# Kernel tuning notes

Measured on AMD Instinct MI355X. Metric: run time of the kernel, lower is better.

Reference implementation:

```python
import jax, jax.numpy as jnp
import numpy as np


def setup_inputs() -> dict:
    key = jax.random.key(0)
    k1, k2 = jax.random.split(key)
    B, N, M = 4, 8192, 8192
    rec = jax.random.normal(k1, (B, N, 3), dtype=jnp.float32)
    data = jax.random.normal(k2, (B, M, 3), dtype=jnp.float32)
    return {"rec": rec, "data": data}


def reference(rec, data):
    # Squared pairwise Euclidean distances: (B, N, M)
    x2 = jnp.sum(rec * rec, axis=-1)          # (B, N)
    y2 = jnp.sum(data * data, axis=-1)        # (B, M)
    xy = jnp.einsum('bnd,bmd->bnm', rec, data)  # (B, N, M)
    d = x2[:, :, None] + y2[:, None, :] - 2.0 * xy
    d = jnp.maximum(d, 0.0)
    rec_dist = jnp.min(d, axis=2)   # (B, N): nearest data point for each rec point
    data_dist = jnp.min(d, axis=1)  # (B, M): nearest rec point for each data point
    # Chamfer: per-batch max of the two directed mean distances, then batch mean
    per_batch = jnp.maximum(jnp.mean(rec_dist, axis=1), jnp.mean(data_dist, axis=1))
    return jnp.mean(per_batch)
```

## Files before the change

kernel.cpp:

```cpp
#include <hip/hip_runtime.h>

typedef float f32x16 __attribute__((ext_vector_type(16)));
typedef short bf16x8 __attribute__((ext_vector_type(8)));

constexpr int SROWS  = 256;
constexpr int NSLICE = 4;

__device__ inline short f2bf(float x) {
    unsigned u = __float_as_uint(x);
    unsigned r = (u + 0x7fffu + ((u >> 16) & 1u)) >> 16;
    return (short)r;
}
__device__ inline float bf2f(short h) {
    return __uint_as_float(((unsigned)(unsigned short)h) << 16);
}
__device__ inline float vmin16(f32x16 v) {
    float a = fminf(fminf(v[0], v[1]), fminf(v[2], v[3]));
    float b = fminf(fminf(v[4], v[5]), fminf(v[6], v[7]));
    float c = fminf(fminf(v[8], v[9]), fminf(v[10], v[11]));
    float d = fminf(fminf(v[12], v[13]), fminf(v[14], v[15]));
    return fminf(fminf(a, b), fminf(c, d));
}

__global__ __launch_bounds__(256)
void chamfer_prep(const float* __restrict__ rec, const float* __restrict__ data,
                  bf16x8* __restrict__ Ar, bf16x8* __restrict__ Br,
                  bf16x8* __restrict__ Ad, bf16x8* __restrict__ Bd,
                  int N, int M, int B)
{
    const int i = blockIdx.x * 256 + threadIdx.x;
    const int tot0 = B * N, tot = tot0 + B * M;
    if (i >= tot) return;
    const short ONE = 0x3F80;
    const bool isRec = i < tot0;
    const int j = isRec ? i : i - tot0;
    const float* p = (isRec ? rec : data) + (size_t)j * 3;
    const float x = p[0], y = p[1], z = p[2];
    const float w = fmaf(x, x, fmaf(y, y, z * z));
    const short hx = f2bf(x), hy = f2bf(y), hz = f2bf(z);
    const float fx = bf2f(hx), fy = bf2f(hy), fz = bf2f(hz);
    const short nhx = f2bf(-2.f * fx), nhy = f2bf(-2.f * fy), nhz = f2bf(-2.f * fz);
    const short nlx = f2bf(-2.f * (x - fx));
    const short nly = f2bf(-2.f * (y - fy));
    const short nlz = f2bf(-2.f * (z - fz));
    const short lx = f2bf(x - fx), ly = f2bf(y - fy), lz = f2bf(z - fz);
    const short wh = f2bf(w);
    const short wl = f2bf(w - bf2f(wh));

    bf16x8 A0 = {nhx, nhy, nhz, nlx, nly, nlz, wh, wl};
    bf16x8 A1 = {nhx, nhy, nhz, ONE, ONE, 0, 0, 0};
    bf16x8 B0 = {hx, hy, hz, hx, hy, hz, ONE, ONE};
    bf16x8 B1 = {lx, ly, lz, wh, wl, 0, 0, 0};

    bf16x8* Adst = (isRec ? Ar : Ad) + 2 * (size_t)j;
    bf16x8* Bdst = (isRec ? Br : Bd) + 2 * (size_t)j;
    Adst[0] = A0; Adst[1] = A1;
    Bdst[0] = B0; Bdst[1] = B1;
}

__global__ __launch_bounds__(256, 4)
void chamfer_mfma_kernel(const bf16x8* __restrict__ Ar, const bf16x8* __restrict__ Bd,
                         const bf16x8* __restrict__ Ad, const bf16x8* __restrict__ Br,
                         float* __restrict__ part_data,
                         float* __restrict__ part_rec,
                         int N, int M, int B)
{
    const int nSB1 = N / SROWS;
    const int G1   = B * nSB1 * NSLICE;

    const bf16x8* Ap; const bf16x8* Bp; float* outp;
    int S, T, idx;
    if ((int)blockIdx.x < G1) {
        Ap = Ar; Bp = Bd; outp = part_data; S = N; T = M; idx = blockIdx.x;
    } else {
        Ap = Ad; Bp = Br; outp = part_rec;  S = M; T = N; idx = blockIdx.x - G1;
    }
    const int nSB = S / SROWS;
    const int sl  = idx % NSLICE; idx /= NSLICE;
    const int sb  = idx % nSB;
    const int b   = idx / nSB;

    const int lane = threadIdx.x & 63, wave = threadIdx.x >> 6;
    const int c = lane & 31, h = lane >> 5;

    const bf16x8* __restrict__ Ab = Ap + 2 * ((size_t)b * S + sb * SROWS);
    const bf16x8* __restrict__ Bb = Bp + 2 * ((size_t)b * T);
    float* __restrict__ outBase = outp + ((size_t)b * nSB + sb) * T;

    bf16x8 a[8];
    #pragma unroll
    for (int f = 0; f < 8; ++f) a[f] = Ab[2 * (f * 32 + c) + h];

    f32x16 zacc;
    #pragma unroll
    for (int r = 0; r < 16; ++r) zacc[r] = 0.f;

    const int TS32 = (T / NSLICE) >> 5;
    const int t0   = sl * TS32 + wave;
    const int tEnd = (sl + 1) * TS32;

    bf16x8 bcur = Bb[2 * ((size_t)t0 * 32 + c) + h];
    for (int t = t0; t < tEnd; t += 4) {
        int tn = t + 4; if (tn >= tEnd) tn = t0;
        bf16x8 bnext = Bb[2 * ((size_t)tn * 32 + c) + h];

        f32x16 d0 = __builtin_amdgcn_mfma_f32_32x32x16_bf16(a[0], bcur, zacc, 0, 0, 0);
        f32x16 d1 = __builtin_amdgcn_mfma_f32_32x32x16_bf16(a[1], bcur, zacc, 0, 0, 0);
        float m0 = fminf(vmin16(d0), vmin16(d1));
        f32x16 d2 = __builtin_amdgcn_mfma_f32_32x32x16_bf16(a[2], bcur, zacc, 0, 0, 0);
        f32x16 d3 = __builtin_amdgcn_mfma_f32_32x32x16_bf16(a[3], bcur, zacc, 0, 0, 0);
        float m1 = fminf(vmin16(d2), vmin16(d3));
        f32x16 d4 = __builtin_amdgcn_mfma_f32_32x32x16_bf16(a[4], bcur, zacc, 0, 0, 0);
        f32x16 d5 = __builtin_amdgcn_mfma_f32_32x32x16_bf16(a[5], bcur, zacc, 0, 0, 0);
        float m2 = fminf(vmin16(d4), vmin16(d5));
        f32x16 d6 = __builtin_amdgcn_mfma_f32_32x32x16_bf16(a[6], bcur, zacc, 0, 0, 0);
        f32x16 d7 = __builtin_amdgcn_mfma_f32_32x32x16_bf16(a[7], bcur, zacc, 0, 0, 0);
        float m3 = fminf(vmin16(d6), vmin16(d7));

        float cm = fminf(fminf(m0, m1), fminf(m2, m3));
        cm = fminf(cm, __shfl_xor(cm, 32));
        if (lane < 32)
            outBase[(size_t)t * 32 + c] = cm;
        bcur = bnext;
    }
}

__global__ __launch_bounds__(256)
void chamfer_stage2(const float* __restrict__ part_data,
                    const float* __restrict__ part_rec,
                    float* __restrict__ bsums, int N, int M, int B)
{
    __shared__ float wsum[4];
    const int gid = blockIdx.x * 256 + threadIdx.x;
    const int nD = B * M;

    const float* base; size_t stride; int depth;
    if (gid < nD) {
        const int b = gid / M, col = gid - b * M;
        base = part_data + ((size_t)b * (N / SROWS)) * M + col;
        stride = M; depth = N / SROWS;
    } else {
        const int g = gid - nD;
        const int b = g / N, col = g - b * N;
        base = part_rec + ((size_t)b * (M / SROWS)) * N + col;
        stride = N; depth = M / SROWS;
    }
    float m0 = 3.4e38f, m1 = 3.4e38f, m2 = 3.4e38f, m3 = 3.4e38f;
    int s = 0;
    for (; s + 4 <= depth; s += 4) {
        m0 = fminf(m0, base[(s + 0) * stride]);
        m1 = fminf(m1, base[(s + 1) * stride]);
        m2 = fminf(m2, base[(s + 2) * stride]);
        m3 = fminf(m3, base[(s + 3) * stride]);
    }
    for (; s < depth; ++s) m0 = fminf(m0, base[s * stride]);
    float d = fmaxf(fminf(fminf(m0, m1), fminf(m2, m3)), 0.f);

    for (int off = 32; off; off >>= 1) d += __shfl_down(d, off);
    if ((threadIdx.x & 63) == 0) wsum[threadIdx.x >> 6] = d;
    __syncthreads();
    if (threadIdx.x == 0)
        bsums[blockIdx.x] = wsum[0] + wsum[1] + wsum[2] + wsum[3];
}

__global__ __launch_bounds__(256)
void chamfer_finalize(const float* __restrict__ bsums, float* __restrict__ out,
                      int N, int M, int B)
{
    __shared__ float smem[512];
    __shared__ float seg[16];
    const int ncD = M >> 8, ncR = N >> 8;
    const int nD  = B * ncD, ntot = nD + B * ncR;
    const int tid = threadIdx.x;
    for (int i = tid; i < ntot; i += 256) smem[i] = bsums[i];
    __syncthreads();
    if (tid < 2 * B) {
        const int dir = tid / B, bb = tid % B;
        float s = 0.f;
        if (dir == 0) for (int i = 0; i < ncD; ++i) s += smem[bb * ncD + i];
        else          for (int i = 0; i < ncR; ++i) s += smem[nD + bb * ncR + i];
        seg[tid] = s;
    }
    __syncthreads();
    if (tid == 0) {
        float acc = 0.f;
        for (int bb = 0; bb < B; ++bb)
            acc += fmaxf(seg[B + bb] / (float)N, seg[bb] / (float)M);
        out[0] = acc / (float)B;
    }
}

extern "C" void kernel_launch(void* const* d_in, const int* in_sizes, int n_in,
                              void* d_out, int out_size, void* d_ws, size_t ws_size,
                              hipStream_t stream)
{
    const float* rec  = (const float*)d_in[0];
    const float* data = (const float*)d_in[1];
    const int B = 4;
    const int N = in_sizes[0] / (B * 3);
    const int M = in_sizes[1] / (B * 3);
    const int tot = B * (N + M);

    char* w = (char*)d_ws;
    bf16x8* Ar = (bf16x8*)w;  w += (size_t)B * N * 2 * sizeof(bf16x8);
    bf16x8* Br = (bf16x8*)w;  w += (size_t)B * N * 2 * sizeof(bf16x8);
    bf16x8* Ad = (bf16x8*)w;  w += (size_t)B * M * 2 * sizeof(bf16x8);
    bf16x8* Bd = (bf16x8*)w;  w += (size_t)B * M * 2 * sizeof(bf16x8);
    float* part_data = (float*)w;  w += (size_t)B * (N / SROWS) * M * sizeof(float);
    float* part_rec  = (float*)w;  w += (size_t)B * (M / SROWS) * N * sizeof(float);
    float* bsums = (float*)w;

    chamfer_prep<<<(tot + 255) / 256, 256, 0, stream>>>(rec, data, Ar, Br, Ad, Bd,
                                                        N, M, B);
    const int G = B * (N / SROWS) * NSLICE + B * (M / SROWS) * NSLICE;
    chamfer_mfma_kernel<<<G, 256, 0, stream>>>(Ar, Bd, Ad, Br,
                                               part_data, part_rec, N, M, B);
    chamfer_stage2<<<tot / 256, 256, 0, stream>>>(part_data, part_rec, bsums,
                                                  N, M, B);
    chamfer_finalize<<<1, 256, 0, stream>>>(bsums, (float*)d_out, N, M, B);
}
```

Measured before the change: 48.60 us.

## Halve row tile and slices, reduce min elementwise before horizontal reduce

Each block now holds 128 source rows (four MFMA A fragments instead of eight) and the target range is split into two slices instead of four. This keeps the grid size unchanged while each wave runs a longer loop with fewer MFMAs per iteration. The min reduction now combines the MFMA outputs elementwise first and then does a single horizontal reduction written as three-input min chains, to cut VALU min work per MFMA. Partial-output writes and stage-2 depth double because there are twice as many source blocks, and each loaded B fragment is reused across fewer A rows.

```diff
diff --git a/kernel.cpp b/kernel.cpp
--- a/kernel.cpp
+++ b/kernel.cpp
@@ -3,8 +3,8 @@
 typedef float f32x16 __attribute__((ext_vector_type(16)));
 typedef short bf16x8 __attribute__((ext_vector_type(8)));
 
-constexpr int SROWS  = 256;
-constexpr int NSLICE = 4;
+constexpr int SROWS  = 128;
+constexpr int NSLICE = 2;
 
 __device__ inline short f2bf(float x) {
     unsigned u = __float_as_uint(x);
@@ -14,12 +14,15 @@
 __device__ inline float bf2f(short h) {
     return __uint_as_float(((unsigned)(unsigned short)h) << 16);
 }
-__device__ inline float vmin16(f32x16 v) {
-    float a = fminf(fminf(v[0], v[1]), fminf(v[2], v[3]));
-    float b = fminf(fminf(v[4], v[5]), fminf(v[6], v[7]));
-    float c = fminf(fminf(v[8], v[9]), fminf(v[10], v[11]));
-    float d = fminf(fminf(v[12], v[13]), fminf(v[14], v[15]));
-    return fminf(fminf(a, b), fminf(c, d));
+__device__ inline float vmin16_t(f32x16 v) {
+    float t1 = fminf(fminf(v[0], v[1]), v[2]);
+    float t2 = fminf(fminf(v[3], v[4]), v[5]);
+    float t3 = fminf(fminf(v[6], v[7]), v[8]);
+    float t4 = fminf(fminf(v[9], v[10]), v[11]);
+    float t5 = fminf(fminf(v[12], v[13]), v[14]);
+    float u1 = fminf(fminf(t1, t2), t3);
+    float u2 = fminf(fminf(t4, t5), v[15]);
+    return fminf(u1, u2);
 }
 
 __global__ __launch_bounds__(256)
@@ -87,9 +90,10 @@
     const bf16x8* __restrict__ Bb = Bp + 2 * ((size_t)b * T);
     float* __restrict__ outBase = outp + ((size_t)b * nSB + sb) * T;
 
-    bf16x8 a[8];
-    #pragma unroll
-    for (int f = 0; f < 8; ++f) a[f] = Ab[2 * (f * 32 + c) + h];
+    bf16x8 a0 = Ab[2 * (0 * 32 + c) + h];
+    bf16x8 a1 = Ab[2 * (1 * 32 + c) + h];
+    bf16x8 a2 = Ab[2 * (2 * 32 + c) + h];
+    bf16x8 a3 = Ab[2 * (3 * 32 + c) + h];
 
     f32x16 zacc;
     #pragma unroll
@@ -104,20 +108,18 @@
         int tn = t + 4; if (tn >= tEnd) tn = t0;
         bf16x8 bnext = Bb[2 * ((size_t)tn * 32 + c) + h];
 
-        f32x16 d0 = __builtin_amdgcn_mfma_f32_32x32x16_bf16(a[0], bcur, zacc, 0, 0, 0);
-        f32x16 d1 = __builtin_amdgcn_mfma_f32_32x32x16_bf16(a[1], bcur, zacc, 0, 0, 0);
-        float m0 = fminf(vmin16(d0), vmin16(d1));
-        f32x16 d2 = __builtin_amdgcn_mfma_f32_32x32x16_bf16(a[2], bcur, zacc, 0, 0, 0);
-        f32x16 d3 = __builtin_amdgcn_mfma_f32_32x32x16_bf16(a[3], bcur, zacc, 0, 0, 0);
-        float m1 = fminf(vmin16(d2), vmin16(d3));
-        f32x16 d4 = __builtin_amdgcn_mfma_f32_32x32x16_bf16(a[4], bcur, zacc, 0, 0, 0);
-        f32x16 d5 = __builtin_amdgcn_mfma_f32_32x32x16_bf16(a[5], bcur, zacc, 0, 0, 0);
-        float m2 = fminf(vmin16(d4), vmin16(d5));
-        f32x16 d6 = __builtin_amdgcn_mfma_f32_32x32x16_bf16(a[6], bcur, zacc, 0, 0, 0);
-        f32x16 d7 = __builtin_amdgcn_mfma_f32_32x32x16_bf16(a[7], bcur, zacc, 0, 0, 0);
-        float m3 = fminf(vmin16(d6), vmin16(d7));
-
-        float cm = fminf(fminf(m0, m1), fminf(m2, m3));
+        f32x16 d0 = __builtin_amdgcn_mfma_f32_32x32x16_bf16(a0, bcur, zacc, 0, 0, 0);
+        f32x16 d1 = __builtin_amdgcn_mfma_f32_32x32x16_bf16(a1, bcur, zacc, 0, 0, 0);
+        f32x16 acc;
+        #pragma unroll
+        for (int r = 0; r < 16; ++r) acc[r] = fminf(d0[r], d1[r]);
+        f32x16 d2 = __builtin_amdgcn_mfma_f32_32x32x16_bf16(a2, bcur, zacc, 0, 0, 0);
+        f32x16 d3 = __builtin_amdgcn_mfma_f32_32x32x16_bf16(a3, bcur, zacc, 0, 0, 0);
+        #pragma unroll
+        for (int r = 0; r < 16; ++r)
+            acc[r] = fminf(fminf(d2[r], d3[r]), acc[r]);
+
+        float cm = vmin16_t(acc);
         cm = fminf(cm, __shfl_xor(cm, 32));
         if (lane < 32)
             outBase[(size_t)t * 32 + c] = cm;
```

Result: slower. 52.67 us (+8.4%).
